# Kernel tuning notes

Hardware: AMD Instinct MI355X
Metric: run time of the kernel (lower is better)

Reference implementation:

```python
import jax, jax.numpy as jnp
import numpy as np

B_GRAPHS, N_NODES = 16, 4096
IN_CH, HID = 256, 512
HEADS, HC = 1, 512  # SGFormerAttention(hidden, heads=1, head_channels=hidden)
NUM_LAYERS = 2
LN_EPS = 1e-5
QK_EPS = 1e-6


def setup_inputs() -> dict:
    key = jax.random.key(0)
    ks = jax.random.split(key, 10)

    def w(k, shape, scale=0.02):
        return jax.random.normal(k, shape, jnp.float32) * scale

    inp = {
        "x": jax.random.normal(ks[0], (B_GRAPHS * N_NODES, IN_CH), jnp.float32),
        "fc0_w": w(ks[1], (HID, IN_CH)),
        "fc0_b": jnp.zeros((HID,), jnp.float32),
        "ln0_g": jnp.ones((HID,), jnp.float32),
        "ln0_b": jnp.zeros((HID,), jnp.float32),
        "q0_w": w(ks[2], (HEADS * HC, HID)),
        "k0_w": w(ks[3], (HEADS * HC, HID)),
        "v0_w": w(ks[4], (HEADS * HC, HID)),
        "ln1_g": jnp.ones((HID,), jnp.float32),
        "ln1_b": jnp.zeros((HID,), jnp.float32),
        "q1_w": w(ks[5], (HEADS * HC, HID)),
        "k1_w": w(ks[6], (HEADS * HC, HID)),
        "v1_w": w(ks[7], (HEADS * HC, HID)),
        "ln2_g": jnp.ones((HID,), jnp.float32),
        "ln2_b": jnp.zeros((HID,), jnp.float32),
        "batch": jnp.repeat(jnp.arange(B_GRAPHS, dtype=jnp.int32), N_NODES),
        "num_graphs": B_GRAPHS,
    }
    return inp


def layernorm(x, g, b):
    mu = x.mean(axis=-1, keepdims=True)
    var = ((x - mu) ** 2).mean(axis=-1, keepdims=True)
    return (x - mu) / jnp.sqrt(var + LN_EPS) * g + b


def sg_attention(x, qw, kw, vw):
    # x: [B, N, HID]; linear (kernelized) global attention, softmax-free.
    B, N, _ = x.shape
    q = (x @ qw.T).reshape(B, N, HEADS, HC)
    k = (x @ kw.T).reshape(B, N, HEADS, HC)
    v = (x @ vw.T).reshape(B, N, HEADS, HC)
    q = jnp.where(q == 0, QK_EPS, q)
    k = jnp.where(k == 0, QK_EPS, k)
    q = q / jnp.linalg.norm(q, axis=-1, keepdims=True)
    k = k / jnp.linalg.norm(k, axis=-1, keepdims=True)
    kvs = jnp.einsum('blhm,blhd->bhmd', k, v)          # [B,H,HC,HC]
    num = jnp.einsum('bnhm,bhmd->bnhd', q, kvs) + N * v
    ks_sum = k.sum(axis=1)                             # [B,H,HC]
    denom = jnp.einsum('bnhm,bhm->bnh', q, ks_sum)[..., None] + float(N)
    return (num / denom).mean(axis=2)                  # [B,N,HC] (mean over heads)


def reference(x, fc0_w, fc0_b, ln0_g, ln0_b,
              q0_w, k0_w, v0_w, ln1_g, ln1_b,
              q1_w, k1_w, v1_w, ln2_g, ln2_b,
              batch, num_graphs):
    total = x.shape[0]
    # stable sort by graph id, remember inverse permutation
    indices = jnp.argsort(batch, stable=True)
    rev_perm = jnp.zeros((total,), jnp.int32).at[indices].set(
        jnp.arange(total, dtype=jnp.int32))
    xs = x[indices]
    # uniform graph sizes -> to_dense_batch is a reshape; mask is all-True
    h = xs.reshape(num_graphs, total // num_graphs, x.shape[1])
    h = h @ fc0_w.T + fc0_b
    h = jax.nn.relu(layernorm(h, ln0_g, ln0_b))  # dropout inactive (eval)
    layers = [h]
    for (qw, kw, vw, g, b) in ((q0_w, k0_w, v0_w, ln1_g, ln1_b),
                               (q1_w, k1_w, v1_w, ln2_g, ln2_b)):
        a = sg_attention(layers[-1], qw, kw, vw)
        a = (a + layers[-1]) / 2.0
        a = jax.nn.relu(layernorm(a, g, b))
        layers.append(a)
    out = layers[-1].reshape(total, -1)
    return out[rev_perm]
```

## Files before the change

kernel.cpp:

```cpp
#include <hip/hip_runtime.h>

#define TNODES 65536
#define NGRAPH 16
#define NNODE  4096
#define INCH   256
#define HID    512

using u16 = unsigned short;
using u32 = unsigned int;
using v8s = __attribute__((ext_vector_type(8))) short;
using v4f = __attribute__((ext_vector_type(4))) float;

__device__ __forceinline__ float bf2f(u16 u) {
    union { u32 i; float f; } v; v.i = ((u32)u) << 16; return v.f;
}
__device__ __forceinline__ u16 f2bf(float f) {
    union { float f; u32 i; } v; v.f = f;
    u32 x = v.i;
    return (u16)((x + 0x7fffu + ((x >> 16) & 1u)) >> 16);
}
__device__ __forceinline__ void up4(uint2 p, float* f) {
    f[0] = __uint_as_float(p.x << 16); f[1] = __uint_as_float(p.x & 0xffff0000u);
    f[2] = __uint_as_float(p.y << 16); f[3] = __uint_as_float(p.y & 0xffff0000u);
}
__device__ __forceinline__ uint2 pk4(float a, float b, float c, float d) {
    uint2 r;
    r.x = (u32)f2bf(a) | ((u32)f2bf(b) << 16);
    r.y = (u32)f2bf(c) | ((u32)f2bf(d) << 16);
    return r;
}

#define MFMA(a, b, c) __builtin_amdgcn_mfma_f32_16x16x32_bf16((a), (b), (c), 0, 0, 0)

#define GLD16(gp, sp) __builtin_amdgcn_global_load_lds( \
    (const __attribute__((address_space(1))) u32*)(const void*)(gp), \
    (__attribute__((address_space(3))) u32*)(void*)(sp), 16, 0, 0)

#define CFENCE() asm volatile("" ::: "memory")

__global__ void k_cvt4(const float* __restrict__ s, u16* __restrict__ d, int n4) {
    for (int i = blockIdx.x * blockDim.x + threadIdx.x; i < n4; i += gridDim.x * blockDim.x) {
        float4 f = ((const float4*)s)[i];
        ((uint2*)d)[i] = pk4(f.x, f.y, f.z, f.w);
    }
}

__global__ void k_zero(float* __restrict__ p, int n) {
    int i = blockIdx.x * 256 + threadIdx.x;
    if (i < n) p[i] = 0.f;
}

__global__ void k_red4(const u16* __restrict__ p, u16* __restrict__ o, int n8) {
    const size_t P = (size_t)NGRAPH * HID * HID;
    for (int i = blockIdx.x * blockDim.x + threadIdx.x; i < n8; i += gridDim.x * blockDim.x) {
        size_t b = (size_t)i * 8;
        float s[8] = {0.f, 0.f, 0.f, 0.f, 0.f, 0.f, 0.f, 0.f};
        #pragma unroll
        for (int ss = 0; ss < 4; ++ss) {
            v8s v = *(const v8s*)(p + ss * P + b);
            const u16* vp = (const u16*)&v;
            #pragma unroll
            for (int j = 0; j < 8; ++j) s[j] += bf2f(vp[j]);
        }
        uint2 lo = pk4(s[0], s[1], s[2], s[3]);
        uint2 hi = pk4(s[4], s[5], s[6], s[7]);
        uint4 w; w.x = lo.x; w.y = lo.y; w.z = hi.x; w.w = hi.y;
        *(uint4*)(o + b) = w;
    }
}

template<int LDK, int KLEN>
__device__ __forceinline__ void gemm_core(const u16* __restrict__ A,
                                          const u16* __restrict__ W,
                                          u16* sA, u16* sW, v4f (&acc)[8][4]) {
    const int t = threadIdx.x, lane = t & 63;
    const int q = lane >> 4, m15 = lane & 15;
    const int w = t >> 6, wr = w >> 2, wc = w & 3;

    #pragma unroll
    for (int n = 0; n < 8; ++n)
        #pragma unroll
        for (int rt = 0; rt < 4; ++rt)
            #pragma unroll
            for (int e = 0; e < 4; ++e) acc[n][rt][e] = 0.f;

    int aoff[4], woff[8];
    #pragma unroll
    for (int rt = 0; rt < 4; ++rt) {
        int r = wr * 64 + rt * 16 + m15;
        aoff[rt] = r * 32 + ((q ^ ((r >> 1) & 3)) * 8);
    }
    #pragma unroll
    for (int n = 0; n < 8; ++n) {
        int r = wc * 128 + n * 16 + m15;
        woff[n] = r * 32 + ((q ^ ((r >> 1) & 3)) * 8);
    }

    auto stage = [&](int k0, int buf) {
        u16* dW = sW + buf * (512 * 32);
        #pragma unroll
        for (int p = 0; p < 4; ++p) {
            int sf = p * 512 + t, row = sf >> 2, sl = sf & 3;
            int gc = k0 + ((sl ^ ((row >> 1) & 3)) * 8);
            GLD16(W + (size_t)row * LDK + gc, dW + sf * 8);
        }
        {
            int row = t >> 2, sl = t & 3;
            int gc = k0 + ((sl ^ ((row >> 1) & 3)) * 8);
            GLD16(A + (size_t)row * LDK + gc, sA + buf * (128 * 32) + t * 8);
        }
    };

    const int KT = KLEN / 32;
    stage(0, 0);
    stage(32, 1);
    int cur = 0;
    for (int kt = 0; kt < KT; ++kt) {
        if (kt + 1 < KT) asm volatile("s_waitcnt vmcnt(5)" ::: "memory");
        else             asm volatile("s_waitcnt vmcnt(0)" ::: "memory");
        __builtin_amdgcn_s_barrier();
        CFENCE();
        __builtin_amdgcn_sched_barrier(0);
        const u16* cA = sA + cur * (128 * 32);
        const u16* cW = sW + cur * (512 * 32);
        v8s b[4];
        #pragma unroll
        for (int rt = 0; rt < 4; ++rt) b[rt] = *(const v8s*)(cA + aoff[rt]);
        #pragma unroll
        for (int n = 0; n < 8; ++n) {
            v8s af = *(const v8s*)(cW + woff[n]);
            #pragma unroll
            for (int rt = 0; rt < 4; ++rt)
                acc[n][rt] = MFMA(af, b[rt], acc[n][rt]);
        }
        CFENCE();
        __builtin_amdgcn_s_barrier();
        CFENCE();
        if (kt + 2 < KT) stage((kt + 2) * 32, cur);
        cur ^= 1;
    }
}


__device__ __forceinline__ int tswz(int c) {
    return (((c >> 2) & 3) << 4) ^ ((c & 3) << 3);
}

__launch_bounds__(512, 2)
__global__ void k_fc(const u16* __restrict__ xb, const u16* __restrict__ wb,
                     const float* __restrict__ bias, const float* __restrict__ lg,
                     const float* __restrict__ lb, u16* __restrict__ h) {
    __shared__ u16 sA[2][128 * 32];
    __shared__ u16 sW[2][512 * 32];
    __shared__ float red[2][128][4];
    __shared__ float rowv[2][128];
    const int t = threadIdx.x, lane = t & 63, w = t >> 6;
    const int q = lane >> 4, m15 = lane & 15;
    const int wr = w >> 2, wc = w & 3;
    const int bx = (int)blockIdx.x;
    const int swz = (bx & 7) * ((int)gridDim.x >> 3) + (bx >> 3);
    const int r0 = swz * 128;
    v4f acc[8][4];
    gemm_core<INCH, INCH>(xb + (size_t)r0 * INCH, wb, &sA[0][0], &sW[0][0], acc);

    float sm[4] = {0.f, 0.f, 0.f, 0.f}, sq[4] = {0.f, 0.f, 0.f, 0.f};
    #pragma unroll
    for (int n = 0; n < 8; ++n) {
        int c = wc * 128 + n * 16 + q * 4;
        float4 bi = *(const float4*)(bias + c);
        const float* bp = &bi.x;
        #pragma unroll
        for (int rt = 0; rt < 4; ++rt)
            #pragma unroll
            for (int e = 0; e < 4; ++e) {
                float a = acc[n][rt][e] + bp[e];
                acc[n][rt][e] = a;
                sm[rt] += a; sq[rt] += a * a;
            }
    }
    #pragma unroll
    for (int rt = 0; rt < 4; ++rt) {
        sm[rt] += __shfl_xor(sm[rt], 16); sm[rt] += __shfl_xor(sm[rt], 32);
        sq[rt] += __shfl_xor(sq[rt], 16); sq[rt] += __shfl_xor(sq[rt], 32);
    }
    if (lane < 16)
        #pragma unroll
        for (int rt = 0; rt < 4; ++rt) {
            red[0][wr * 64 + rt * 16 + m15][wc] = sm[rt];
            red[1][wr * 64 + rt * 16 + m15][wc] = sq[rt];
        }
    __syncthreads();
    if (t < 128) {
        float tt = red[0][t][0] + red[0][t][1] + red[0][t][2] + red[0][t][3];
        float t2 = red[1][t][0] + red[1][t][1] + red[1][t][2] + red[1][t][3];
        float mu = tt * (1.f / HID);
        float rs = rsqrtf(t2 * (1.f / HID) - mu * mu + 1e-5f);
        rowv[0][t] = mu; rowv[1][t] = rs;
    }
    __syncthreads();
    #pragma unroll
    for (int n = 0; n < 8; ++n) {
        int c = wc * 128 + n * 16 + q * 4;
        float4 g4 = *(const float4*)(lg + c);
        float4 b4 = *(const float4*)(lb + c);
        #pragma unroll
        for (int rt = 0; rt < 4; ++rt) {
            int row = wr * 64 + rt * 16 + m15;
            float mu = rowv[0][row], rs = rowv[1][row];
            float v0 = (acc[n][rt][0] - mu) * rs * g4.x + b4.x;
            float v1 = (acc[n][rt][1] - mu) * rs * g4.y + b4.y;
            float v2 = (acc[n][rt][2] - mu) * rs * g4.z + b4.z;
            float v3 = (acc[n][rt][3] - mu) * rs * g4.w + b4.w;
            v0 = v0 > 0.f ? v0 : 0.f; v1 = v1 > 0.f ? v1 : 0.f;
            v2 = v2 > 0.f ? v2 : 0.f; v3 = v3 > 0.f ? v3 : 0.f;
            *(uint2*)&h[(size_t)(r0 + row) * HID + c] = pk4(v0, v1, v2, v3);
        }
    }
}

__launch_bounds__(512, 2)
__global__ void k_proj(const u16* __restrict__ hsrc, const u16* __restrict__ wkb,
                       const u16* __restrict__ wvb, u16* __restrict__ kt,
                       u16* __restrict__ vt, float* __restrict__ vo,
                       float* __restrict__ ksum) {
    __shared__ u16 sA[2][128 * 32];
    __shared__ u16 sW[2][512 * 32];
    __shared__ float red[128][4];
    __shared__ float rowv[128];
    u16* sT = &sW[0][0];
    const int t = threadIdx.x, lane = t & 63, w = t >> 6;
    const int q = lane >> 4, m15 = lane & 15;
    const int wr = w >> 2, wc = w & 3;
    const int bx = (int)blockIdx.x;
    const int swz = (bx & 7) * ((int)gridDim.x >> 3) + (bx >> 3);
    const int r0 = swz * 128;
    const int g = swz >> 5;
    const int lbase = (swz & 31) * 128;
    const int mode = blockIdx.y;
    v4f acc[8][4];
    gemm_core<HID, HID>(hsrc + (size_t)r0 * HID, mode ? wvb : wkb,
                        &sA[0][0], &sW[0][0], acc);

    const int ch = t;
    const int xs = (((ch >> 2) & 3) << 1) ^ (ch & 3);
    if (mode == 0) {
        float sq[4] = {0.f, 0.f, 0.f, 0.f};
        #pragma unroll
        for (int n = 0; n < 8; ++n)
            #pragma unroll
            for (int rt = 0; rt < 4; ++rt)
                #pragma unroll
                for (int e = 0; e < 4; ++e) {
                    float vv = acc[n][rt][e];
                    if (vv == 0.f) vv = 1e-6f;
                    acc[n][rt][e] = vv;
                    sq[rt] += vv * vv;
                }
        #pragma unroll
        for (int rt = 0; rt < 4; ++rt) {
            sq[rt] += __shfl_xor(sq[rt], 16); sq[rt] += __shfl_xor(sq[rt], 32);
        }
        if (lane < 16)
            #pragma unroll
            for (int rt = 0; rt < 4; ++rt)
                red[wr * 64 + rt * 16 + m15][wc] = sq[rt];
        __syncthreads();
        if (t < 128)
            rowv[t] = rsqrtf(red[t][0] + red[t][1] + red[t][2] + red[t][3]);
        __syncthreads();
        float sum = 0.f;
        #pragma unroll
        for (int pass = 0; pass < 2; ++pass) {
            if (wr == pass) {
                #pragma unroll
                for (int n = 0; n < 8; ++n)
                    #pragma unroll
                    for (int rt = 0; rt < 4; ++rt) {
                        int rl = rt * 16 + m15;
                        float rn = rowv[wr * 64 + rl];
                        #pragma unroll
                        for (int e = 0; e < 4; ++e) {
                            int c = wc * 128 + n * 16 + q * 4 + e;
                            sT[(c << 6) + (rl ^ tswz(c))] = f2bf(acc[n][rt][e] * rn);
                        }
                    }
            }
            __syncthreads();
            u16* op = kt + ((size_t)(g * 512 + ch)) * NNODE + lbase + pass * 64;
            #pragma unroll
            for (int jj = 0; jj < 8; ++jj) {
                v8s cvec = *(const v8s*)&sT[(ch << 6) + jj * 8];
                int l0 = (jj ^ xs) * 8;
                *(v8s*)(op + l0) = cvec;
                const u16* cp = (const u16*)&cvec;
                #pragma unroll
                for (int i = 0; i < 8; ++i) sum += bf2f(cp[i]);
            }
            __syncthreads();
        }
        atomicAdd(&ksum[g * 512 + ch], sum);
    } else {
        #pragma unroll
        for (int n = 0; n < 8; ++n) {
            int c = wc * 128 + n * 16 + q * 4;
            #pragma unroll
            for (int rt = 0; rt < 4; ++rt) {
                int row = wr * 64 + rt * 16 + m15;
                float4 o = {acc[n][rt][0], acc[n][rt][1], acc[n][rt][2], acc[n][rt][3]};
                *(float4*)&vo[(size_t)(r0 + row) * HID + c] = o;
            }
        }
        #pragma unroll
        for (int pass = 0; pass < 2; ++pass) {
            if (wr == pass) {
                #pragma unroll
                for (int n = 0; n < 8; ++n)
                    #pragma unroll
                    for (int rt = 0; rt < 4; ++rt) {
                        int rl = rt * 16 + m15;
                        #pragma unroll
                        for (int e = 0; e < 4; ++e) {
                            int c = wc * 128 + n * 16 + q * 4 + e;
                            sT[(c << 6) + (rl ^ tswz(c))] = f2bf(acc[n][rt][e]);
                        }
                    }
            }
            __syncthreads();
            u16* op = vt + ((size_t)(g * 512 + ch)) * NNODE + lbase + pass * 64;
            #pragma unroll
            for (int jj = 0; jj < 8; ++jj) {
                v8s cvec = *(const v8s*)&sT[(ch << 6) + jj * 8];
                int l0 = (jj ^ xs) * 8;
                *(v8s*)(op + l0) = cvec;
            }
            __syncthreads();
        }
    }
}

__launch_bounds__(512, 2)
__global__ void k_kvmm2(const u16* __restrict__ kt, const u16* __restrict__ vt,
                        u16* __restrict__ kvp) {
    __shared__ u16 sA[2][128 * 32];
    __shared__ u16 sW[2][512 * 32];
    const int t = threadIdx.x, lane = t & 63, w = t >> 6;
    const int q = lane >> 4, m15 = lane & 15;
    const int wr = w >> 2, wc = w & 3;
    const int bx = (int)blockIdx.x;
    const int swz = (bx & 7) * 32 + (bx >> 3);
    const int db = swz & 3, s = (swz >> 2) & 3, g = swz >> 4;
    const u16* A = vt + ((size_t)(g * 512 + db * 128)) * NNODE + s * 1024;
    const u16* W = kt + ((size_t)(g * 512)) * NNODE + s * 1024;
    v4f acc[8][4];
    gemm_core<NNODE, 1024>(A, W, &sA[0][0], &sW[0][0], acc);
    u16* plane = kvp + (size_t)s * NGRAPH * HID * HID;
    #pragma unroll
    for (int n = 0; n < 8; ++n) {
        int m = wc * 128 + n * 16 + q * 4;
        #pragma unroll
        for (int rt = 0; rt < 4; ++rt) {
            int d = db * 128 + wr * 64 + rt * 16 + m15;
            *(uint2*)&plane[((size_t)(g * 512) + d) * 512 + m] =
                pk4(acc[n][rt][0], acc[n][rt][1], acc[n][rt][2], acc[n][rt][3]);
        }
    }
}

__launch_bounds__(512, 2)
__global__ void k_qnorm(const u16* __restrict__ hsrc, const u16* __restrict__ qwb,
                        const float* __restrict__ ks, u16* __restrict__ qo,
                        float* __restrict__ dnv) {
    __shared__ u16 sA[2][128 * 32];
    __shared__ u16 sW[2][512 * 32];
    __shared__ float red[2][128][4];
    __shared__ float rowv[128];
    const int t = threadIdx.x, lane = t & 63, w = t >> 6;
    const int q = lane >> 4, m15 = lane & 15;
    const int wr = w >> 2, wc = w & 3;
    const int bx = (int)blockIdx.x;
    const int swz = (bx & 7) * ((int)gridDim.x >> 3) + (bx >> 3);
    const int r0 = swz * 128;
    const int gi = swz >> 5;
    v4f acc[8][4];
    gemm_core<HID, HID>(hsrc + (size_t)r0 * HID, qwb, &sA[0][0], &sW[0][0], acc);

    float ss[4] = {0.f, 0.f, 0.f, 0.f}, ws[4] = {0.f, 0.f, 0.f, 0.f};
    #pragma unroll
    for (int n = 0; n < 8; ++n) {
        int c = wc * 128 + n * 16 + q * 4;
        float4 kv = *(const float4*)(ks + (gi << 9) + c);
        const float* kp = &kv.x;
        #pragma unroll
        for (int rt = 0; rt < 4; ++rt)
            #pragma unroll
            for (int e = 0; e < 4; ++e) {
                float vv = acc[n][rt][e];
                if (vv == 0.f) vv = 1e-6f;
                acc[n][rt][e] = vv;
                ss[rt] += vv * vv; ws[rt] += vv * kp[e];
            }
    }
    #pragma unroll
    for (int rt = 0; rt < 4; ++rt) {
        ss[rt] += __shfl_xor(ss[rt], 16); ss[rt] += __shfl_xor(ss[rt], 32);
        ws[rt] += __shfl_xor(ws[rt], 16); ws[rt] += __shfl_xor(ws[rt], 32);
    }
    if (lane < 16)
        #pragma unroll
        for (int rt = 0; rt < 4; ++rt) {
            red[0][wr * 64 + rt * 16 + m15][wc] = ss[rt];
            red[1][wr * 64 + rt * 16 + m15][wc] = ws[rt];
        }
    __syncthreads();
    if (t < 128) {
        float st = red[0][t][0] + red[0][t][1] + red[0][t][2] + red[0][t][3];
        float wt = red[1][t][0] + red[1][t][1] + red[1][t][2] + red[1][t][3];
        float rn = rsqrtf(st);
        rowv[t] = rn;
        dnv[r0 + t] = 1.f / (rn * wt + (float)NNODE);
    }
    __syncthreads();
    #pragma unroll
    for (int n = 0; n < 8; ++n) {
        int c = wc * 128 + n * 16 + q * 4;
        #pragma unroll
        for (int rt = 0; rt < 4; ++rt) {
            int row = wr * 64 + rt * 16 + m15;
            float rn = rowv[row];
            *(uint2*)&qo[(size_t)(r0 + row) * HID + c] =
                pk4(acc[n][rt][0] * rn, acc[n][rt][1] * rn,
                    acc[n][rt][2] * rn, acc[n][rt][3] * rn);
        }
    }
}

__launch_bounds__(512, 2)
__global__ void k_attn2(const u16* __restrict__ qhat, const u16* __restrict__ kvstb,
                        const float* __restrict__ dnv, const float* __restrict__ vsrc,
                        const u16* __restrict__ hsrc, const float* __restrict__ lg,
                        const float* __restrict__ lb, u16* __restrict__ outb,
                        float* __restrict__ outf) {
    __shared__ u16 sA[2][128 * 32];
    __shared__ u16 sW[2][512 * 32];
    __shared__ float red[2][128][4];
    __shared__ float rowv[2][128];
    const int t = threadIdx.x, lane = t & 63, w = t >> 6;
    const int q = lane >> 4, m15 = lane & 15;
    const int wr = w >> 2, wc = w & 3;
    const int bx = (int)blockIdx.x;
    const int swz = (bx & 7) * ((int)gridDim.x >> 3) + (bx >> 3);
    const int r0 = swz * 128;
    const int gi = swz >> 5;
    v4f acc[8][4];
    gemm_core<HID, HID>(qhat + (size_t)r0 * HID, kvstb + (size_t)gi * HID * HID,
                        &sA[0][0], &sW[0][0], acc);

    float dv[4];
    #pragma unroll
    for (int rt = 0; rt < 4; ++rt) dv[rt] = dnv[r0 + wr * 64 + rt * 16 + m15];
    float sm[4] = {0.f, 0.f, 0.f, 0.f}, sq[4] = {0.f, 0.f, 0.f, 0.f};
    #pragma unroll
    for (int n = 0; n < 8; ++n) {
        int c = wc * 128 + n * 16 + q * 4;
        #pragma unroll
        for (int rt = 0; rt < 4; ++rt) {
            int row = wr * 64 + rt * 16 + m15;
            size_t og = (size_t)(r0 + row) * HID + c;
            float hh[4]; up4(*(const uint2*)&hsrc[og], hh);
            float4 vv = *(const float4*)&vsrc[og];
            const float* vp = &vv.x;
            #pragma unroll
            for (int e = 0; e < 4; ++e) {
                float a = ((acc[n][rt][e] + (float)NNODE * vp[e]) * dv[rt] + hh[e]) * 0.5f;
                acc[n][rt][e] = a;
                sm[rt] += a; sq[rt] += a * a;
            }
        }
    }
    #pragma unroll
    for (int rt = 0; rt < 4; ++rt) {
        sm[rt] += __shfl_xor(sm[rt], 16); sm[rt] += __shfl_xor(sm[rt], 32);
        sq[rt] += __shfl_xor(sq[rt], 16); sq[rt] += __shfl_xor(sq[rt], 32);
    }
    if (lane < 16)
        #pragma unroll
        for (int rt = 0; rt < 4; ++rt) {
            red[0][wr * 64 + rt * 16 + m15][wc] = sm[rt];
            red[1][wr * 64 + rt * 16 + m15][wc] = sq[rt];
        }
    __syncthreads();
    if (t < 128) {
        float tt = red[0][t][0] + red[0][t][1] + red[0][t][2] + red[0][t][3];
        float t2 = red[1][t][0] + red[1][t][1] + red[1][t][2] + red[1][t][3];
        float mu = tt * (1.f / HID);
        float rs = rsqrtf(t2 * (1.f / HID) - mu * mu + 1e-5f);
        rowv[0][t] = mu; rowv[1][t] = rs;
    }
    __syncthreads();
    #pragma unroll
    for (int n = 0; n < 8; ++n) {
        int c = wc * 128 + n * 16 + q * 4;
        float4 g4 = *(const float4*)(lg + c);
        float4 b4 = *(const float4*)(lb + c);
        #pragma unroll
        for (int rt = 0; rt < 4; ++rt) {
            int row = wr * 64 + rt * 16 + m15;
            float mu = rowv[0][row], rs = rowv[1][row];
            float v0 = (acc[n][rt][0] - mu) * rs * g4.x + b4.x;
            float v1 = (acc[n][rt][1] - mu) * rs * g4.y + b4.y;
            float v2 = (acc[n][rt][2] - mu) * rs * g4.z + b4.z;
            float v3 = (acc[n][rt][3] - mu) * rs * g4.w + b4.w;
            v0 = v0 > 0.f ? v0 : 0.f; v1 = v1 > 0.f ? v1 : 0.f;
            v2 = v2 > 0.f ? v2 : 0.f; v3 = v3 > 0.f ? v3 : 0.f;
            size_t og = (size_t)(r0 + row) * HID + c;
            if (outf) {
                float4 o = {v0, v1, v2, v3};
                *(float4*)&outf[og] = o;
            } else {
                *(uint2*)&outb[og] = pk4(v0, v1, v2, v3);
            }
        }
    }
}

extern "C" void kernel_launch(void* const* d_in, const int* in_sizes, int n_in,
                              void* d_out, int out_size, void* d_ws, size_t ws_size,
                              hipStream_t stream) {
    const float* x    = (const float*)d_in[0];
    const float* fc0w = (const float*)d_in[1];
    const float* fc0b = (const float*)d_in[2];
    const float* ln0g = (const float*)d_in[3];
    const float* ln0b = (const float*)d_in[4];
    const float* q0w  = (const float*)d_in[5];
    const float* k0w  = (const float*)d_in[6];
    const float* v0w  = (const float*)d_in[7];
    const float* ln1g = (const float*)d_in[8];
    const float* ln1b = (const float*)d_in[9];
    const float* q1w  = (const float*)d_in[10];
    const float* k1w  = (const float*)d_in[11];
    const float* v1w  = (const float*)d_in[12];
    const float* ln2g = (const float*)d_in[13];
    const float* ln2b = (const float*)d_in[14];

    const size_t M64 = (size_t)TNODES * HID * 2;
    const size_t PL  = (size_t)NGRAPH * HID * HID * 2;
    char* wsc = (char*)d_ws;
    u16*   H   = (u16*)wsc;
    u16*   Kt  = (u16*)(wsc + M64);
    u16*   Vt  = (u16*)(wsc + 2 * M64);
    u16*   KVp = (u16*)(wsc + 3 * M64);
    u16*   KVb = (u16*)(wsc + 3 * M64 + 4 * PL);
    float* KS  = (float*)(wsc + 3 * M64 + 5 * PL);
    float* DNV = KS + NGRAPH * HID;
    u16*   Wc  = (u16*)((char*)DNV + (size_t)TNODES * sizeof(float));
    u16* fc0wb = Wc;
    u16* q0b = Wc + 131072;
    u16* k0b = Wc + 393216;
    u16* v0b = Wc + 655360;
    u16* q1b = Wc + 917504;
    u16* k1b = Wc + 1179648;
    u16* v1b = Wc + 1441792;
    u16* Xb  = Vt;
    u16* QH  = Vt;
    float* V = (float*)d_out;

    dim3 b256(256), b512(512);
    k_cvt4<<<dim3(64),  b256, 0, stream>>>(fc0w, fc0wb, HID * INCH / 4);
    k_cvt4<<<dim3(64),  b256, 0, stream>>>(q0w, q0b, HID * HID / 4);
    k_cvt4<<<dim3(64),  b256, 0, stream>>>(k0w, k0b, HID * HID / 4);
    k_cvt4<<<dim3(64),  b256, 0, stream>>>(v0w, v0b, HID * HID / 4);
    k_cvt4<<<dim3(64),  b256, 0, stream>>>(q1w, q1b, HID * HID / 4);
    k_cvt4<<<dim3(64),  b256, 0, stream>>>(k1w, k1b, HID * HID / 4);
    k_cvt4<<<dim3(64),  b256, 0, stream>>>(v1w, v1b, HID * HID / 4);
    k_cvt4<<<dim3(1024), b256, 0, stream>>>(x, Xb, TNODES * INCH / 4);

    k_fc<<<dim3(TNODES / 128), b512, 0, stream>>>(Xb, fc0wb, fc0b, ln0g, ln0b, H);

    k_zero<<<dim3(32), b256, 0, stream>>>(KS, NGRAPH * HID);
    k_proj<<<dim3(TNODES / 128, 2), b512, 0, stream>>>(H, k0b, v0b, Kt, Vt, V, KS);
    k_kvmm2<<<dim3(256), b512, 0, stream>>>(Kt, Vt, KVp);
    k_red4<<<dim3(2048), b256, 0, stream>>>(KVp, KVb, NGRAPH * HID * HID / 8);
    k_qnorm<<<dim3(TNODES / 128), b512, 0, stream>>>(H, q0b, KS, QH, DNV);
    k_attn2<<<dim3(TNODES / 128), b512, 0, stream>>>(QH, KVb, DNV, V, H, ln1g, ln1b,
                                                     H, nullptr);

    k_zero<<<dim3(32), b256, 0, stream>>>(KS, NGRAPH * HID);
    k_proj<<<dim3(TNODES / 128, 2), b512, 0, stream>>>(H, k1b, v1b, Kt, Vt, V, KS);
    k_kvmm2<<<dim3(256), b512, 0, stream>>>(Kt, Vt, KVp);
    k_red4<<<dim3(2048), b256, 0, stream>>>(KVp, KVb, NGRAPH * HID * HID / 8);
    k_qnorm<<<dim3(TNODES / 128), b512, 0, stream>>>(H, q1b, KS, QH, DNV);
    k_attn2<<<dim3(TNODES / 128), b512, 0, stream>>>(QH, KVb, DNV, V, H, ln2g, ln2b,
                                                     nullptr, (float*)d_out);
}
```

Measured before the change: 1.034 ms.

## Drop fp32 V buffer and read transposed bf16 V in attention epilogue

The projection kernel no longer writes a separate fp32 copy of V. The attention epilogue instead reads V from the transposed bf16 buffer that the KV matmul already uses, and Q-hat is moved to the K buffer so V stays live. All kernels also switch to one aliased shared-memory block to cut LDS footprint. This removes a 128 MB fp32 write plus read per layer, at the cost of strided 2-byte gathers from the transposed layout and the use of bf16-rounded V in the residual term.

```diff
diff --git a/kernel.cpp b/kernel.cpp
--- a/kernel.cpp
+++ b/kernel.cpp
@@ -146,14 +146,19 @@
     return (((c >> 2) & 3) << 4) ^ ((c & 3) << 3);
 }
 
+#define SMEM_DECL __shared__ char smem[81920]
+#define SA ((u16*)smem)
+#define SW ((u16*)(smem + 16384))
+
 __launch_bounds__(512, 2)
 __global__ void k_fc(const u16* __restrict__ xb, const u16* __restrict__ wb,
                      const float* __restrict__ bias, const float* __restrict__ lg,
                      const float* __restrict__ lb, u16* __restrict__ h) {
-    __shared__ u16 sA[2][128 * 32];
-    __shared__ u16 sW[2][512 * 32];
-    __shared__ float red[2][128][4];
-    __shared__ float rowv[2][128];
+    SMEM_DECL;
+    float (*redA)[4] = (float(*)[4])smem;
+    float (*redB)[4] = (float(*)[4])(smem + 2048);
+    float* mu_s = (float*)(smem + 4096);
+    float* rs_s = (float*)(smem + 4608);
     const int t = threadIdx.x, lane = t & 63, w = t >> 6;
     const int q = lane >> 4, m15 = lane & 15;
     const int wr = w >> 2, wc = w & 3;
@@ -161,7 +166,7 @@
     const int swz = (bx & 7) * ((int)gridDim.x >> 3) + (bx >> 3);
     const int r0 = swz * 128;
     v4f acc[8][4];
-    gemm_core<INCH, INCH>(xb + (size_t)r0 * INCH, wb, &sA[0][0], &sW[0][0], acc);
+    gemm_core<INCH, INCH>(xb + (size_t)r0 * INCH, wb, SA, SW, acc);
 
     float sm[4] = {0.f, 0.f, 0.f, 0.f}, sq[4] = {0.f, 0.f, 0.f, 0.f};
     #pragma unroll
@@ -186,16 +191,16 @@
     if (lane < 16)
         #pragma unroll
         for (int rt = 0; rt < 4; ++rt) {
-            red[0][wr * 64 + rt * 16 + m15][wc] = sm[rt];
-            red[1][wr * 64 + rt * 16 + m15][wc] = sq[rt];
+            redA[wr * 64 + rt * 16 + m15][wc] = sm[rt];
+            redB[wr * 64 + rt * 16 + m15][wc] = sq[rt];
         }
     __syncthreads();
     if (t < 128) {
-        float tt = red[0][t][0] + red[0][t][1] + red[0][t][2] + red[0][t][3];
-        float t2 = red[1][t][0] + red[1][t][1] + red[1][t][2] + red[1][t][3];
+        float tt = redA[t][0] + redA[t][1] + redA[t][2] + redA[t][3];
+        float t2 = redB[t][0] + redB[t][1] + redB[t][2] + redB[t][3];
         float mu = tt * (1.f / HID);
         float rs = rsqrtf(t2 * (1.f / HID) - mu * mu + 1e-5f);
-        rowv[0][t] = mu; rowv[1][t] = rs;
+        mu_s[t] = mu; rs_s[t] = rs;
     }
     __syncthreads();
     #pragma unroll
@@ -206,7 +211,7 @@
         #pragma unroll
         for (int rt = 0; rt < 4; ++rt) {
             int row = wr * 64 + rt * 16 + m15;
-            float mu = rowv[0][row], rs = rowv[1][row];
+            float mu = mu_s[row], rs = rs_s[row];
             float v0 = (acc[n][rt][0] - mu) * rs * g4.x + b4.x;
             float v1 = (acc[n][rt][1] - mu) * rs * g4.y + b4.y;
             float v2 = (acc[n][rt][2] - mu) * rs * g4.z + b4.z;
@@ -221,13 +226,11 @@
 __launch_bounds__(512, 2)
 __global__ void k_proj(const u16* __restrict__ hsrc, const u16* __restrict__ wkb,
                        const u16* __restrict__ wvb, u16* __restrict__ kt,
-                       u16* __restrict__ vt, float* __restrict__ vo,
-                       float* __restrict__ ksum) {
-    __shared__ u16 sA[2][128 * 32];
-    __shared__ u16 sW[2][512 * 32];
-    __shared__ float red[128][4];
-    __shared__ float rowv[128];
-    u16* sT = &sW[0][0];
+                       u16* __restrict__ vt, float* __restrict__ ksum) {
+    SMEM_DECL;
+    float (*red)[4] = (float(*)[4])smem;
+    float* rowv = (float*)(smem + 2048);
+    u16* sT = SW;
     const int t = threadIdx.x, lane = t & 63, w = t >> 6;
     const int q = lane >> 4, m15 = lane & 15;
     const int wr = w >> 2, wc = w & 3;
@@ -238,8 +241,7 @@
     const int lbase = (swz & 31) * 128;
     const int mode = blockIdx.y;
     v4f acc[8][4];
-    gemm_core<HID, HID>(hsrc + (size_t)r0 * HID, mode ? wvb : wkb,
-                        &sA[0][0], &sW[0][0], acc);
+    gemm_core<HID, HID>(hsrc + (size_t)r0 * HID, mode ? wvb : wkb, SA, SW, acc);
 
     const int ch = t;
     const int xs = (((ch >> 2) & 3) << 1) ^ (ch & 3);
@@ -301,16 +303,6 @@
         atomicAdd(&ksum[g * 512 + ch], sum);
     } else {
         #pragma unroll
-        for (int n = 0; n < 8; ++n) {
-            int c = wc * 128 + n * 16 + q * 4;
-            #pragma unroll
-            for (int rt = 0; rt < 4; ++rt) {
-                int row = wr * 64 + rt * 16 + m15;
-                float4 o = {acc[n][rt][0], acc[n][rt][1], acc[n][rt][2], acc[n][rt][3]};
-                *(float4*)&vo[(size_t)(r0 + row) * HID + c] = o;
-            }
-        }
-        #pragma unroll
         for (int pass = 0; pass < 2; ++pass) {
             if (wr == pass) {
                 #pragma unroll
@@ -341,8 +333,7 @@
 __launch_bounds__(512, 2)
 __global__ void k_kvmm2(const u16* __restrict__ kt, const u16* __restrict__ vt,
                         u16* __restrict__ kvp) {
-    __shared__ u16 sA[2][128 * 32];
-    __shared__ u16 sW[2][512 * 32];
+    SMEM_DECL;
     const int t = threadIdx.x, lane = t & 63, w = t >> 6;
     const int q = lane >> 4, m15 = lane & 15;
     const int wr = w >> 2, wc = w & 3;
@@ -352,7 +343,7 @@
     const u16* A = vt + ((size_t)(g * 512 + db * 128)) * NNODE + s * 1024;
     const u16* W = kt + ((size_t)(g * 512)) * NNODE + s * 1024;
     v4f acc[8][4];
-    gemm_core<NNODE, 1024>(A, W, &sA[0][0], &sW[0][0], acc);
+    gemm_core<NNODE, 1024>(A, W, SA, SW, acc);
     u16* plane = kvp + (size_t)s * NGRAPH * HID * HID;
     #pragma unroll
     for (int n = 0; n < 8; ++n) {
@@ -370,10 +361,10 @@
 __global__ void k_qnorm(const u16* __restrict__ hsrc, const u16* __restrict__ qwb,
                         const float* __restrict__ ks, u16* __restrict__ qo,
                         float* __restrict__ dnv) {
-    __shared__ u16 sA[2][128 * 32];
-    __shared__ u16 sW[2][512 * 32];
-    __shared__ float red[2][128][4];
-    __shared__ float rowv[128];
+    SMEM_DECL;
+    float (*redA)[4] = (float(*)[4])smem;
+    float (*redB)[4] = (float(*)[4])(smem + 2048);
+    float* rowv = (float*)(smem + 4096);
     const int t = threadIdx.x, lane = t & 63, w = t >> 6;
     const int q = lane >> 4, m15 = lane & 15;
     const int wr = w >> 2, wc = w & 3;
@@ -382,7 +373,7 @@
     const int r0 = swz * 128;
     const int gi = swz >> 5;
     v4f acc[8][4];
-    gemm_core<HID, HID>(hsrc + (size_t)r0 * HID, qwb, &sA[0][0], &sW[0][0], acc);
+    gemm_core<HID, HID>(hsrc + (size_t)r0 * HID, qwb, SA, SW, acc);
 
     float ss[4] = {0.f, 0.f, 0.f, 0.f}, ws[4] = {0.f, 0.f, 0.f, 0.f};
     #pragma unroll
@@ -408,13 +399,13 @@
     if (lane < 16)
         #pragma unroll
         for (int rt = 0; rt < 4; ++rt) {
-            red[0][wr * 64 + rt * 16 + m15][wc] = ss[rt];
-            red[1][wr * 64 + rt * 16 + m15][wc] = ws[rt];
+            redA[wr * 64 + rt * 16 + m15][wc] = ss[rt];
+            redB[wr * 64 + rt * 16 + m15][wc] = ws[rt];
         }
     __syncthreads();
     if (t < 128) {
-        float st = red[0][t][0] + red[0][t][1] + red[0][t][2] + red[0][t][3];
-        float wt = red[1][t][0] + red[1][t][1] + red[1][t][2] + red[1][t][3];
+        float st = redA[t][0] + redA[t][1] + redA[t][2] + redA[t][3];
+        float wt = redB[t][0] + redB[t][1] + redB[t][2] + redB[t][3];
         float rn = rsqrtf(st);
         rowv[t] = rn;
         dnv[r0 + t] = 1.f / (rn * wt + (float)NNODE);
@@ -436,14 +427,15 @@
 
 __launch_bounds__(512, 2)
 __global__ void k_attn2(const u16* __restrict__ qhat, const u16* __restrict__ kvstb,
-                        const float* __restrict__ dnv, const float* __restrict__ vsrc,
+                        const float* __restrict__ dnv, const u16* __restrict__ vt,
                         const u16* __restrict__ hsrc, const float* __restrict__ lg,
                         const float* __restrict__ lb, u16* __restrict__ outb,
                         float* __restrict__ outf) {
-    __shared__ u16 sA[2][128 * 32];
-    __shared__ u16 sW[2][512 * 32];
-    __shared__ float red[2][128][4];
-    __shared__ float rowv[2][128];
+    SMEM_DECL;
+    float (*redA)[4] = (float(*)[4])smem;
+    float (*redB)[4] = (float(*)[4])(smem + 2048);
+    float* mu_s = (float*)(smem + 4096);
+    float* rs_s = (float*)(smem + 4608);
     const int t = threadIdx.x, lane = t & 63, w = t >> 6;
     const int q = lane >> 4, m15 = lane & 15;
     const int wr = w >> 2, wc = w & 3;
@@ -453,25 +445,26 @@
     const int gi = swz >> 5;
     v4f acc[8][4];
     gemm_core<HID, HID>(qhat + (size_t)r0 * HID, kvstb + (size_t)gi * HID * HID,
-                        &sA[0][0], &sW[0][0], acc);
+                        SA, SW, acc);
 
     float dv[4];
     #pragma unroll
     for (int rt = 0; rt < 4; ++rt) dv[rt] = dnv[r0 + wr * 64 + rt * 16 + m15];
+    const u16* vtg = vt + (size_t)(gi * 512) * NNODE + ((swz & 31) * 128 + wr * 64 + m15);
     float sm[4] = {0.f, 0.f, 0.f, 0.f}, sq[4] = {0.f, 0.f, 0.f, 0.f};
     #pragma unroll
     for (int n = 0; n < 8; ++n) {
         int c = wc * 128 + n * 16 + q * 4;
+        const u16* vb = vtg + (size_t)c * NNODE;
         #pragma unroll
         for (int rt = 0; rt < 4; ++rt) {
             int row = wr * 64 + rt * 16 + m15;
             size_t og = (size_t)(r0 + row) * HID + c;
             float hh[4]; up4(*(const uint2*)&hsrc[og], hh);
-            float4 vv = *(const float4*)&vsrc[og];
-            const float* vp = &vv.x;
             #pragma unroll
             for (int e = 0; e < 4; ++e) {
-                float a = ((acc[n][rt][e] + (float)NNODE * vp[e]) * dv[rt] + hh[e]) * 0.5f;
+                float vv = bf2f(vb[(size_t)e * NNODE + rt * 16]);
+                float a = ((acc[n][rt][e] + (float)NNODE * vv) * dv[rt] + hh[e]) * 0.5f;
                 acc[n][rt][e] = a;
                 sm[rt] += a; sq[rt] += a * a;
             }
@@ -485,16 +478,16 @@
     if (lane < 16)
         #pragma unroll
         for (int rt = 0; rt < 4; ++rt) {
-            red[0][wr * 64 + rt * 16 + m15][wc] = sm[rt];
-            red[1][wr * 64 + rt * 16 + m15][wc] = sq[rt];
+            redA[wr * 64 + rt * 16 + m15][wc] = sm[rt];
+            redB[wr * 64 + rt * 16 + m15][wc] = sq[rt];
         }
     __syncthreads();
     if (t < 128) {
-        float tt = red[0][t][0] + red[0][t][1] + red[0][t][2] + red[0][t][3];
-        float t2 = red[1][t][0] + red[1][t][1] + red[1][t][2] + red[1][t][3];
+        float tt = redA[t][0] + redA[t][1] + redA[t][2] + redA[t][3];
+        float t2 = redB[t][0] + redB[t][1] + redB[t][2] + redB[t][3];
         float mu = tt * (1.f / HID);
         float rs = rsqrtf(t2 * (1.f / HID) - mu * mu + 1e-5f);
-        rowv[0][t] = mu; rowv[1][t] = rs;
+        mu_s[t] = mu; rs_s[t] = rs;
     }
     __syncthreads();
     #pragma unroll
@@ -505,7 +498,7 @@
         #pragma unroll
         for (int rt = 0; rt < 4; ++rt) {
             int row = wr * 64 + rt * 16 + m15;
-            float mu = rowv[0][row], rs = rowv[1][row];
+            float mu = mu_s[row], rs = rs_s[row];
             float v0 = (acc[n][rt][0] - mu) * rs * g4.x + b4.x;
             float v1 = (acc[n][rt][1] - mu) * rs * g4.y + b4.y;
             float v2 = (acc[n][rt][2] - mu) * rs * g4.z + b4.z;
@@ -561,8 +554,7 @@
     u16* k1b = Wc + 1179648;
     u16* v1b = Wc + 1441792;
     u16* Xb  = Vt;
-    u16* QH  = Vt;
-    float* V = (float*)d_out;
+    u16* QH  = Kt;
 
     dim3 b256(256), b512(512);
     k_cvt4<<<dim3(64),  b256, 0, stream>>>(fc0w, fc0wb, HID * INCH / 4);
@@ -577,18 +569,18 @@
     k_fc<<<dim3(TNODES / 128), b512, 0, stream>>>(Xb, fc0wb, fc0b, ln0g, ln0b, H);
 
     k_zero<<<dim3(32), b256, 0, stream>>>(KS, NGRAPH * HID);
-    k_proj<<<dim3(TNODES / 128, 2), b512, 0, stream>>>(H, k0b, v0b, Kt, Vt, V, KS);
+    k_proj<<<dim3(TNODES / 128, 2), b512, 0, stream>>>(H, k0b, v0b, Kt, Vt, KS);
     k_kvmm2<<<dim3(256), b512, 0, stream>>>(Kt, Vt, KVp);
     k_red4<<<dim3(2048), b256, 0, stream>>>(KVp, KVb, NGRAPH * HID * HID / 8);
     k_qnorm<<<dim3(TNODES / 128), b512, 0, stream>>>(H, q0b, KS, QH, DNV);
-    k_attn2<<<dim3(TNODES / 128), b512, 0, stream>>>(QH, KVb, DNV, V, H, ln1g, ln1b,
+    k_attn2<<<dim3(TNODES / 128), b512, 0, stream>>>(QH, KVb, DNV, Vt, H, ln1g, ln1b,
                                                      H, nullptr);
 
     k_zero<<<dim3(32), b256, 0, stream>>>(KS, NGRAPH * HID);
-    k_proj<<<dim3(TNODES / 128, 2), b512, 0, stream>>>(H, k1b, v1b, Kt, Vt, V, KS);
+    k_proj<<<dim3(TNODES / 128, 2), b512, 0, stream>>>(H, k1b, v1b, Kt, Vt, KS);
     k_kvmm2<<<dim3(256), b512, 0, stream>>>(Kt, Vt, KVp);
     k_red4<<<dim3(2048), b256, 0, stream>>>(KVp, KVb, NGRAPH * HID * HID / 8);
     k_qnorm<<<dim3(TNODES / 128), b512, 0, stream>>>(H, q1b, KS, QH, DNV);
-    k_attn2<<<dim3(TNODES / 128), b512, 0, stream>>>(QH, KVb, DNV, V, H, ln2g, ln2b,
+    k_attn2<<<dim3(TNODES / 128), b512, 0, stream>>>(QH, KVb, DNV, Vt, H, ln2g, ln2b,
                                                      nullptr, (float*)d_out);
 }
```

After: 909.7 us. -12.0%, faster.
